# Optimization experiments

Measured on AMD Instinct MI355X. Metric: run time of the kernel, lower is better.

## Reference

```python
import jax, jax.numpy as jnp
import numpy as np

K = 512
H = 8

def setup_inputs() -> dict:
    key = jax.random.key(0)
    ks = jax.random.split(key, 6)
    b, t, k = 4, 2048, K
    scale = 1.0 / np.sqrt(k)
    return {
        "x": jax.random.normal(ks[0], (b, t, k), dtype=jnp.float32),
        "Wq": jax.random.normal(ks[1], (k, k), dtype=jnp.float32) * scale,
        "Wk": jax.random.normal(ks[2], (k, k), dtype=jnp.float32) * scale,
        "Wv": jax.random.normal(ks[3], (k, k), dtype=jnp.float32) * scale,
        "Wo": jax.random.normal(ks[4], (k, k), dtype=jnp.float32) * scale,
        "bo": jax.random.normal(ks[5], (k,), dtype=jnp.float32) * 0.01,
    }

def reference(x, Wq, Wk, Wv, Wo, bo):
    b, t, k = x.shape
    h = H
    s = k // h
    # nn.Linear: y = x @ W.T ; weights stored [out, in]
    q = (x @ Wq.T).reshape(b, t, h, s)
    kk = (x @ Wk.T).reshape(b, t, h, s)
    v = (x @ Wv.T).reshape(b, t, h, s)
    # scores: note original divides by sqrt(k) (full model dim), not sqrt(s)
    dot = jnp.einsum("bqhs,bkhs->bhqk", q, kk) / jnp.sqrt(jnp.float32(k))
    attn = jax.nn.softmax(dot, axis=-1)
    out = jnp.einsum("bhqk,bkhs->bqhs", attn, v).reshape(b, t, k)
    return out @ Wo.T + bo
```

## Files before the change

kernel.cpp:

```cpp
#include <hip/hip_runtime.h>

typedef _Float16 f16;
typedef _Float16 f16x8 __attribute__((ext_vector_type(8)));
typedef _Float16 f16x4 __attribute__((ext_vector_type(4)));
typedef float    f32x4 __attribute__((ext_vector_type(4)));
typedef __fp16   fp16x2 __attribute__((ext_vector_type(2)));

#define MFMA(a,b,c) __builtin_amdgcn_mfma_f32_16x16x32_f16((a),(b),(c),0,0,0)

#if __has_builtin(__builtin_amdgcn_exp2f)
#define EXP2(x) __builtin_amdgcn_exp2f(x)
#else
#define EXP2(x) exp2f(x)
#endif

__device__ __forceinline__ void gl_lds16(const void* g, void* l) {
  __builtin_amdgcn_global_load_lds(
      (__attribute__((address_space(1))) void*)(void*)(g),
      (__attribute__((address_space(3))) void*)(l),
      16, 0, 0);
}

__device__ __forceinline__ int SWZ(int row) {
  return ((row & 3) | ((row >> 1) & 4)) << 4;
}

__global__ __launch_bounds__(256) void k_convert(
    const float* __restrict__ x, const float* __restrict__ Wq,
    const float* __restrict__ Wk, const float* __restrict__ Wv,
    const float* __restrict__ Wo,
    f16* __restrict__ x_h, f16* __restrict__ wqkv_h, f16* __restrict__ wo_h) {
  const int XQ    = (8192 * 512) / 4;
  const int WQKVQ = (1536 * 512) / 4;
  const int WOQ   = (512 * 512) / 4;
  const int total = XQ + WQKVQ + WOQ;
  for (int q = blockIdx.x * blockDim.x + threadIdx.x; q < total;
       q += gridDim.x * blockDim.x) {
    const float* src;
    f16* dst;
    if (q < XQ) {
      src = x + q * 4;
      dst = x_h + q * 4;
    } else if (q < XQ + WQKVQ) {
      int j  = q - XQ;
      int r  = j >> 7;
      int c0 = (j & 127) * 4;
      const float* w = (r < 512) ? Wq : (r < 1024) ? Wk : Wv;
      src = w + (r & 511) * 512 + c0;
      dst = wqkv_h + j * 4;
    } else {
      int j = q - XQ - WQKVQ;
      src = Wo + j * 4;
      dst = wo_h + j * 4;
    }
    float4 v = *(const float4*)src;
    f16x4 o = {(f16)v.x, (f16)v.y, (f16)v.z, (f16)v.w};
    *(f16x4*)dst = o;
  }
}

__device__ __forceinline__ void gemm_core(const f16* __restrict__ A,
                                          const f16* __restrict__ B,
                                          int bm, int bn, f32x4 (&acc)[4][4]) {
  __shared__ f16 As[2][128 * 64];
  __shared__ f16 Bs[2][128 * 64];
  const int tid  = threadIdx.x;
  const int lane = tid & 63;
  const int w    = tid >> 6;
  const int wr   = (w >> 1) & 1, wc = w & 1;
  const int r0   = tid >> 3;
  const int cb   = (tid & 7) << 4;

  auto stage = [&](int buf, int kt) {
#pragma unroll
    for (int inst = 0; inst < 4; ++inst) {
      const int row  = inst * 32 + r0;
      const int csrc = cb ^ ((row & 7) << 4);
      gl_lds16(A + (bm + row) * 512 + kt + (csrc >> 1),
               (char*)As[buf] + inst * 4096 + w * 1024);
      gl_lds16(B + (bn + row) * 512 + kt + (csrc >> 1),
               (char*)Bs[buf] + inst * 4096 + w * 1024);
    }
  };

  stage(0, 0);
#pragma unroll
  for (int t = 0; t < 8; ++t) {
    const int cur = t & 1;
    asm volatile("s_waitcnt vmcnt(0)" ::: "memory");
    __builtin_amdgcn_s_barrier();
    __builtin_amdgcn_sched_barrier(0);
    if (t < 7) stage(cur ^ 1, (t + 1) * 64);
    f16x8 af[4][2], bf[4][2];
#pragma unroll
    for (int i = 0; i < 4; ++i) {
      const int ra = wr * 64 + i * 16 + (lane & 15);
      const int rb = wc * 64 + i * 16 + (lane & 15);
#pragma unroll
      for (int ks = 0; ks < 2; ++ks) {
        const int cc = ks * 64 + ((lane >> 4) << 4);
        af[i][ks] = *(const f16x8*)((const char*)As[cur] + ra * 128 + (cc ^ ((ra & 7) << 4)));
        bf[i][ks] = *(const f16x8*)((const char*)Bs[cur] + rb * 128 + (cc ^ ((rb & 7) << 4)));
      }
    }
    __builtin_amdgcn_s_setprio(1);
#pragma unroll
    for (int i = 0; i < 4; ++i)
#pragma unroll
      for (int j = 0; j < 4; ++j) {
        acc[i][j] = MFMA(af[i][0], bf[j][0], acc[i][j]);
        acc[i][j] = MFMA(af[i][1], bf[j][1], acc[i][j]);
      }
    __builtin_amdgcn_s_setprio(0);
  }
}

__global__ __launch_bounds__(256) void k_gemm_qkv(
    const f16* __restrict__ A, const f16* __restrict__ B,
    f16* __restrict__ q_h, f16* __restrict__ k_h, f16* __restrict__ vt_h) {
  const int bm = blockIdx.x * 128;
  const int bn = blockIdx.y * 128;
  f32x4 acc[4][4] = {};
  gemm_core(A, B, bm, bn, acc);

  const int tid  = threadIdx.x;
  const int lane = tid & 63;
  const int w    = tid >> 6;
  const int wr   = (w >> 1) & 1, wc = w & 1;
  const float qscale = 0.044194173824159216f * 1.4426950408889634f;
#pragma unroll
  for (int i = 0; i < 4; ++i) {
    const int m0 = bm + wr * 64 + i * 16 + ((lane >> 4) << 2);
#pragma unroll
    for (int j = 0; j < 4; ++j) {
      const int n   = bn + wc * 64 + j * 16 + (lane & 15);
      const int sec = n >> 9;
      const int nn  = n & 511;
      const int h   = nn >> 6, s = nn & 63;
#pragma unroll
      for (int r = 0; r < 4; ++r) {
        const int m = m0 + r;
        const int b = m >> 11, t = m & 2047;
        const int bh = b * 8 + h;
        const float v = acc[i][j][r];
        if (sec == 0)
          q_h[(bh * 2048 + t) * 64 + s] = (f16)(v * qscale);
        else if (sec == 1)
          k_h[(bh * 2048 + t) * 64 + s] = (f16)v;
        else
          vt_h[(bh * 64 + s) * 2048 + t] = (f16)v;
      }
    }
  }
}

__global__ __launch_bounds__(256) void k_attn(
    const f16* __restrict__ q_h, const f16* __restrict__ k_h,
    const f16* __restrict__ vt_h, f16* __restrict__ a_h) {
  __shared__ f16 Ks[4][64 * 64];
  __shared__ f16 Vs[4][64 * 64];

  const int tid  = threadIdx.x;
  const int lane = tid & 63;
  const int w    = tid >> 6;

  int id = blockIdx.x;
  id = (id & 7) * 64 + (id >> 3);
  const int qt = (id & 15) * 128;
  const int bh = id >> 4;

  const f16* qb = q_h + (size_t)bh * 2048 * 64;
  const f16* kb = k_h + (size_t)bh * 2048 * 64;
  const f16* vb = vt_h + (size_t)bh * 64 * 2048;

  f16x8 qf[2][2];
#pragma unroll
  for (int i = 0; i < 2; ++i) {
    const int qrow = qt + w * 32 + i * 16 + (lane & 15);
#pragma unroll
    for (int ks = 0; ks < 2; ++ks)
      qf[i][ks] = *(const f16x8*)(qb + qrow * 64 + ks * 32 + ((lane >> 4) << 3));
  }

  f32x4 oacc[2][4] = {};
  f32x4 lrun[2]    = {};

  const int r0  = tid >> 3;
  const int cbb = (tid & 7) << 4;

  const f16 one = (f16)1.0f;
  const f16x8 ones = {one, one, one, one, one, one, one, one};

  auto stage = [&](int buf, int ktv) {
#pragma unroll
    for (int inst = 0; inst < 2; ++inst) {
      const int row  = inst * 32 + r0;
      const int csrc = cbb ^ SWZ(row);
      gl_lds16(kb + (ktv + row) * 64 + (csrc >> 1),
               (char*)Ks[buf] + inst * 4096 + w * 1024);
      gl_lds16(vb + row * 2048 + ktv + (csrc >> 1),
               (char*)Vs[buf] + inst * 4096 + w * 1024);
    }
  };

  auto pack4 = [](float a, float b, float c, float d) -> unsigned long long {
    union { fp16x2 h2[2]; unsigned long long u; } t;
    t.h2[0] = __builtin_amdgcn_cvt_pkrtz(a, b);
    t.h2[1] = __builtin_amdgcn_cvt_pkrtz(c, d);
    return t.u;
  };

  auto tile = [&](const f16* ksb, const f16* vsb) {
    f16x8 kf[4][2];
    const int m  = lane & 15;
    const int hi = lane >> 4;
#pragma unroll
    for (int n = 0; n < 4; ++n) {
      const int row = ((n >> 1) << 5) + ((m >> 2) << 3) + ((n & 1) << 2) + (m & 3);
      const int sw  = SWZ(row);
#pragma unroll
      for (int ks = 0; ks < 2; ++ks) {
        const int c = (ks * 64 + (hi << 4)) ^ sw;
        kf[n][ks] = *(const f16x8*)((const char*)ksb + row * 128 + c);
      }
    }
    f32x4 sf[2][4];
    __builtin_amdgcn_s_setprio(1);
#pragma unroll
    for (int i = 0; i < 2; ++i)
#pragma unroll
      for (int n = 0; n < 4; ++n) {
        f32x4 s = {0.f, 0.f, 0.f, 0.f};
        s = MFMA(kf[n][0], qf[i][0], s);
        s = MFMA(kf[n][1], qf[i][1], s);
        sf[i][n] = s;
      }
    __builtin_amdgcn_s_setprio(0);
    f16x8 pa[2][2];
#pragma unroll
    for (int i = 0; i < 2; ++i)
#pragma unroll
      for (int ks = 0; ks < 2; ++ks) {
        union { unsigned long long u[2]; f16x8 v; } u;
        u.u[0] = pack4(EXP2(sf[i][2 * ks][0]), EXP2(sf[i][2 * ks][1]),
                       EXP2(sf[i][2 * ks][2]), EXP2(sf[i][2 * ks][3]));
        u.u[1] = pack4(EXP2(sf[i][2 * ks + 1][0]), EXP2(sf[i][2 * ks + 1][1]),
                       EXP2(sf[i][2 * ks + 1][2]), EXP2(sf[i][2 * ks + 1][3]));
        pa[i][ks] = u.v;
      }
    __builtin_amdgcn_s_setprio(1);
#pragma unroll
    for (int i = 0; i < 2; ++i) {
      lrun[i] = MFMA(pa[i][0], ones, lrun[i]);
      lrun[i] = MFMA(pa[i][1], ones, lrun[i]);
    }
#pragma unroll
    for (int n = 0; n < 4; ++n) {
      const int row = n * 16 + m;
      const int sw  = SWZ(row);
      const f16x8 vf0 = *(const f16x8*)((const char*)vsb + row * 128 + ((hi << 4) ^ sw));
      const f16x8 vf1 = *(const f16x8*)((const char*)vsb + row * 128 + ((64 + (hi << 4)) ^ sw));
#pragma unroll
      for (int i = 0; i < 2; ++i) {
        oacc[i][n] = MFMA(pa[i][0], vf0, oacc[i][n]);
        oacc[i][n] = MFMA(pa[i][1], vf1, oacc[i][n]);
      }
    }
    __builtin_amdgcn_s_setprio(0);
  };

  stage(0, 0);
  stage(1, 64);
  for (int j = 0; j < 16; ++j) {
    const int base = (j & 1) << 1;
    asm volatile("s_waitcnt vmcnt(0)" ::: "memory");
    __builtin_amdgcn_s_barrier();
    __builtin_amdgcn_sched_barrier(0);
    if (j < 15) {
      stage(base ^ 2, (2 * j + 2) * 64);
      stage((base ^ 2) + 1, (2 * j + 3) * 64);
    }
    tile(Ks[base], Vs[base]);
    tile(Ks[base + 1], Vs[base + 1]);
  }

  const int b = bh >> 3, h = bh & 7;
#pragma unroll
  for (int i = 0; i < 2; ++i) {
    float rl[4];
#pragma unroll
    for (int r = 0; r < 4; ++r) rl[r] = 1.0f / lrun[i][r];
#pragma unroll
    for (int n = 0; n < 4; ++n)
#pragma unroll
      for (int r = 0; r < 4; ++r) {
        const int qrow = qt + w * 32 + i * 16 + ((lane >> 4) << 2) + r;
        const int scol = n * 16 + (lane & 15);
        a_h[(size_t)(b * 2048 + qrow) * 512 + h * 64 + scol] =
            (f16)(oacc[i][n][r] * rl[r]);
      }
  }
}

__global__ __launch_bounds__(256) void k_gemm_out(
    const f16* __restrict__ A, const f16* __restrict__ B,
    const float* __restrict__ bo, float* __restrict__ out) {
  const int bm = blockIdx.x * 128;
  const int bn = blockIdx.y * 128;
  f32x4 acc[4][4] = {};
  gemm_core(A, B, bm, bn, acc);

  const int tid  = threadIdx.x;
  const int lane = tid & 63;
  const int w    = tid >> 6;
  const int wr   = (w >> 1) & 1, wc = w & 1;
#pragma unroll
  for (int i = 0; i < 4; ++i) {
    const int m0 = bm + wr * 64 + i * 16 + ((lane >> 4) << 2);
#pragma unroll
    for (int j = 0; j < 4; ++j) {
      const int n = bn + wc * 64 + j * 16 + (lane & 15);
      const float bias = bo[n];
#pragma unroll
      for (int r = 0; r < 4; ++r)
        out[(size_t)(m0 + r) * 512 + n] = acc[i][j][r] + bias;
    }
  }
}

extern "C" void kernel_launch(void* const* d_in, const int* in_sizes, int n_in,
                              void* d_out, int out_size, void* d_ws, size_t ws_size,
                              hipStream_t stream) {
  const float* x  = (const float*)d_in[0];
  const float* Wq = (const float*)d_in[1];
  const float* Wk = (const float*)d_in[2];
  const float* Wv = (const float*)d_in[3];
  const float* Wo = (const float*)d_in[4];
  const float* bo = (const float*)d_in[5];
  float* out = (float*)d_out;

  char* ws = (char*)d_ws;
  f16* x_h    = (f16*)(ws);
  f16* wqkv_h = (f16*)(ws + 8388608);
  f16* wo_h   = (f16*)(ws + 9961472);
  f16* q_h    = (f16*)(ws + 10485760);
  f16* k_h    = (f16*)(ws + 18874368);
  f16* vt_h   = (f16*)(ws + 27262976);
  f16* a_h    = (f16*)(ws + 35651584);
  (void)ws_size; (void)in_sizes; (void)n_in; (void)out_size;

  k_convert<<<2048, 256, 0, stream>>>(x, Wq, Wk, Wv, Wo, x_h, wqkv_h, wo_h);
  k_gemm_qkv<<<dim3(64, 12), 256, 0, stream>>>(x_h, wqkv_h, q_h, k_h, vt_h);
  k_attn<<<512, 256, 0, stream>>>(q_h, k_h, vt_h, a_h);
  k_gemm_out<<<dim3(64, 4), 256, 0, stream>>>(a_h, wo_h, bo, out);
}
```

Baseline: 89.99 us.

## Split attention KV sequence across two wave groups and merge partial outputs in LDS

The attention kernel now launches 512 threads per block, split into two groups of four waves. Each group processes half of the key/value sequence with its own double-buffered LDS staging. The two partial output accumulators and row sums are then combined through shared memory before normalization. This doubles the waves available per query tile to hide latency, but adds a reduction step, extra LDS traffic and barriers, and raises register pressure under the new launch bounds. The softmax max subtraction is still absent, so merging by plain summation stays valid.

```diff
diff --git a/kernel.cpp b/kernel.cpp
--- a/kernel.cpp
+++ b/kernel.cpp
@@ -154,15 +154,16 @@
   }
 }
 
-__global__ __launch_bounds__(256) void k_attn(
+__global__ __launch_bounds__(512, 4) void k_attn(
     const f16* __restrict__ q_h, const f16* __restrict__ k_h,
     const f16* __restrict__ vt_h, f16* __restrict__ a_h) {
-  __shared__ f16 Ks[4][64 * 64];
-  __shared__ f16 Vs[4][64 * 64];
+  __shared__ char smem[65536];
 
   const int tid  = threadIdx.x;
   const int lane = tid & 63;
   const int w    = tid >> 6;
+  const int g    = w >> 2;
+  const int wg   = w & 3;
 
   int id = blockIdx.x;
   id = (id & 7) * 64 + (id >> 3);
@@ -173,10 +174,13 @@
   const f16* kb = k_h + (size_t)bh * 2048 * 64;
   const f16* vb = vt_h + (size_t)bh * 64 * 2048;
 
+  auto KsP = [&](int grp, int buf) { return smem + (grp * 2 + buf) * 8192; };
+  auto VsP = [&](int grp, int buf) { return smem + 32768 + (grp * 2 + buf) * 8192; };
+
   f16x8 qf[2][2];
 #pragma unroll
   for (int i = 0; i < 2; ++i) {
-    const int qrow = qt + w * 32 + i * 16 + (lane & 15);
+    const int qrow = qt + wg * 32 + i * 16 + (lane & 15);
 #pragma unroll
     for (int ks = 0; ks < 2; ++ks)
       qf[i][ks] = *(const f16x8*)(qb + qrow * 64 + ks * 32 + ((lane >> 4) << 3));
@@ -185,21 +189,23 @@
   f32x4 oacc[2][4] = {};
   f32x4 lrun[2]    = {};
 
-  const int r0  = tid >> 3;
+  const int gt  = tid & 255;
+  const int r0  = gt >> 3;
   const int cbb = (tid & 7) << 4;
 
   const f16 one = (f16)1.0f;
   const f16x8 ones = {one, one, one, one, one, one, one, one};
 
-  auto stage = [&](int buf, int ktv) {
+  auto stage = [&](int buf, int t) {
+    const int ktv = g * 1024 + t * 64;
 #pragma unroll
     for (int inst = 0; inst < 2; ++inst) {
       const int row  = inst * 32 + r0;
       const int csrc = cbb ^ SWZ(row);
       gl_lds16(kb + (ktv + row) * 64 + (csrc >> 1),
-               (char*)Ks[buf] + inst * 4096 + w * 1024);
+               KsP(g, buf) + inst * 4096 + wg * 1024);
       gl_lds16(vb + row * 2048 + ktv + (csrc >> 1),
-               (char*)Vs[buf] + inst * 4096 + w * 1024);
+               VsP(g, buf) + inst * 4096 + wg * 1024);
     }
   };
 
@@ -210,7 +216,7 @@
     return t.u;
   };
 
-  auto tile = [&](const f16* ksb, const f16* vsb) {
+  auto tile = [&](const char* ksb, const char* vsb) {
     f16x8 kf[4][2];
     const int m  = lane & 15;
     const int hi = lane >> 4;
@@ -221,7 +227,7 @@
 #pragma unroll
       for (int ks = 0; ks < 2; ++ks) {
         const int c = (ks * 64 + (hi << 4)) ^ sw;
-        kf[n][ks] = *(const f16x8*)((const char*)ksb + row * 128 + c);
+        kf[n][ks] = *(const f16x8*)(ksb + row * 128 + c);
       }
     }
     f32x4 sf[2][4];
@@ -258,8 +264,8 @@
     for (int n = 0; n < 4; ++n) {
       const int row = n * 16 + m;
       const int sw  = SWZ(row);
-      const f16x8 vf0 = *(const f16x8*)((const char*)vsb + row * 128 + ((hi << 4) ^ sw));
-      const f16x8 vf1 = *(const f16x8*)((const char*)vsb + row * 128 + ((64 + (hi << 4)) ^ sw));
+      const f16x8 vf0 = *(const f16x8*)(vsb + row * 128 + ((hi << 4) ^ sw));
+      const f16x8 vf1 = *(const f16x8*)(vsb + row * 128 + ((64 + (hi << 4)) ^ sw));
 #pragma unroll
       for (int i = 0; i < 2; ++i) {
         oacc[i][n] = MFMA(pa[i][0], vf0, oacc[i][n]);
@@ -270,34 +276,47 @@
   };
 
   stage(0, 0);
-  stage(1, 64);
   for (int j = 0; j < 16; ++j) {
-    const int base = (j & 1) << 1;
+    const int cur = j & 1;
     asm volatile("s_waitcnt vmcnt(0)" ::: "memory");
     __builtin_amdgcn_s_barrier();
     __builtin_amdgcn_sched_barrier(0);
-    if (j < 15) {
-      stage(base ^ 2, (2 * j + 2) * 64);
-      stage((base ^ 2) + 1, (2 * j + 3) * 64);
-    }
-    tile(Ks[base], Vs[base]);
-    tile(Ks[base + 1], Vs[base + 1]);
-  }
-
-  const int b = bh >> 3, h = bh & 7;
-#pragma unroll
-  for (int i = 0; i < 2; ++i) {
-    float rl[4];
-#pragma unroll
-    for (int r = 0; r < 4; ++r) rl[r] = 1.0f / lrun[i][r];
-#pragma unroll
-    for (int n = 0; n < 4; ++n)
+    if (j < 15) stage(cur ^ 1, j + 1);
+    tile(KsP(g, cur), VsP(g, cur));
+  }
+
+  __syncthreads();
+  float* Ol = (float*)smem;
+  float* ll = (float*)(smem + 34816);
+
+  if (g == 1) {
+#pragma unroll
+    for (int i = 0; i < 2; ++i)
 #pragma unroll
       for (int r = 0; r < 4; ++r) {
-        const int qrow = qt + w * 32 + i * 16 + ((lane >> 4) << 2) + r;
-        const int scol = n * 16 + (lane & 15);
-        a_h[(size_t)(b * 2048 + qrow) * 512 + h * 64 + scol] =
-            (f16)(oacc[i][n][r] * rl[r]);
+        const int q = wg * 32 + i * 16 + ((lane >> 4) << 2) + r;
+#pragma unroll
+        for (int n = 0; n < 4; ++n)
+          Ol[q * 68 + n * 16 + (lane & 15)] = oacc[i][n][r];
+        if ((lane & 15) == 0) ll[q] = lrun[i][r];
+      }
+  }
+  __syncthreads();
+  if (g == 0) {
+    const int b2 = bh >> 3, h2 = bh & 7;
+#pragma unroll
+    for (int i = 0; i < 2; ++i)
+#pragma unroll
+      for (int r = 0; r < 4; ++r) {
+        const int q  = wg * 32 + i * 16 + ((lane >> 4) << 2) + r;
+        const float rl = 1.0f / (lrun[i][r] + ll[q]);
+        const int qrow = qt + q;
+#pragma unroll
+        for (int n = 0; n < 4; ++n) {
+          const int s = n * 16 + (lane & 15);
+          const float o = oacc[i][n][r] + Ol[q * 68 + s];
+          a_h[(size_t)(b2 * 2048 + qrow) * 512 + h2 * 64 + s] = (f16)(o * rl);
+        }
       }
   }
 }
@@ -351,6 +370,6 @@
 
   k_convert<<<2048, 256, 0, stream>>>(x, Wq, Wk, Wv, Wo, x_h, wqkv_h, wo_h);
   k_gemm_qkv<<<dim3(64, 12), 256, 0, stream>>>(x_h, wqkv_h, q_h, k_h, vt_h);
-  k_attn<<<512, 256, 0, stream>>>(q_h, k_h, vt_h, a_h);
+  k_attn<<<512, 512, 0, stream>>>(q_h, k_h, vt_h, a_h);
   k_gemm_out<<<dim3(64, 4), 256, 0, stream>>>(a_h, wo_h, bo, out);
 }
```

Measured after the change: 86.31 us. 4.1% less time.
